# Performance work log

Hardware: AMD Instinct MI355X
Metric: run time of the kernel (lower is better)

Reference implementation:

```python
import jax, jax.numpy as jnp
import numpy as np
import math

HIDDEN = 1024
HEADS = 16
HEAD_DIM = HIDDEN // HEADS


def setup_inputs() -> dict:
    key = jax.random.key(0)
    k1, k2, k3, k4, k5 = jax.random.split(key, 5)
    B, S = 2, 2048
    scale = 1.0 / math.sqrt(HIDDEN)
    return {
        "batch_hidden": jax.random.normal(k1, (B, S, HIDDEN), dtype=jnp.float32),
        # nn.Linear weights are [out, in]; y = x @ W.T
        "Wq": jax.random.uniform(k2, (HIDDEN, HIDDEN), jnp.float32, -scale, scale),
        "Wk": jax.random.uniform(k3, (HIDDEN, HIDDEN), jnp.float32, -scale, scale),
        "Wg": jax.random.uniform(k4, (HIDDEN, HIDDEN), jnp.float32, -scale, scale),
        "bg": jax.random.uniform(k5, (HIDDEN,), jnp.float32, -scale, scale),
    }


def _split_heads(x):
    # [B,S,H] -> [B,heads,S,head_dim]
    B, S, _ = x.shape
    return x.reshape(B, S, HEADS, HEAD_DIM).transpose(0, 2, 1, 3)


def reference(batch_hidden, Wq, Wk, Wg, bg):
    # NOTE: faithful to source — value uses the KEY projection weights.
    q = batch_hidden @ Wq.T
    k = batch_hidden @ Wk.T
    v = batch_hidden @ Wk.T
    gate = jax.nn.sigmoid(batch_hidden @ Wg.T + bg)  # [B,S,H]

    q = _split_heads(q)  # [B,h,S,d]
    k = _split_heads(k)
    v = _split_heads(v)

    # source: scores = K @ Q^T (softmax over query positions)
    scores = jnp.einsum("bhkd,bhqd->bhkq", k, q) / math.sqrt(HEAD_DIM)
    attn = jax.nn.softmax(scores, axis=-1)  # [B,h,S,S]

    ctx = jnp.einsum("bhkq,bhqd->bhkd", attn, v)  # [B,h,S,d]
    ctx = ctx.transpose(0, 2, 1, 3).reshape(batch_hidden.shape)  # [B,S,H]

    out = gate * ctx
    return out, attn
```

## Files before the change

kernel.cpp:

```cpp
#include <hip/hip_runtime.h>
#include <hip/hip_bf16.h>

#define HID 1024
#define NHEADS 16
#define HDIM 64
#define SEQ 2048
#define NTOK 4096

typedef __attribute__((ext_vector_type(8))) short short8;
typedef __attribute__((ext_vector_type(4))) float f32x4;
typedef unsigned short ush;

__device__ __forceinline__ ush f2bf(float f) {
    unsigned int u = __float_as_uint(f);
    u = (u + 0x7fffu + ((u >> 16) & 1u)) >> 16;
    return (ush)u;
}
__device__ __forceinline__ void async_copy16(const void* g, void* l) {
    __builtin_amdgcn_global_load_lds(
        (const __attribute__((address_space(1))) void*)g,
        (__attribute__((address_space(3))) void*)l, 16, 0, 0);
}
#define SBAR()  __builtin_amdgcn_s_barrier()
#define SCHED() __builtin_amdgcn_sched_barrier(0)

__global__ __launch_bounds__(256) void cvt_kernel(
    const float* __restrict__ X, const float* __restrict__ Wq,
    const float* __restrict__ Wk, const float* __restrict__ Wg,
    ush* __restrict__ Xbf, ush* __restrict__ Wbf)
{
    long i = (long)blockIdx.x * 256 + threadIdx.x;
    const float* src; ush* dst; long j;
    if (i < 524288)      { src = X;  dst = Xbf;           j = i; }
    else if (i < 655360) { src = Wq; dst = Wbf;           j = i - 524288; }
    else if (i < 786432) { src = Wk; dst = Wbf + 1048576; j = i - 655360; }
    else                 { src = Wg; dst = Wbf + 2097152; j = i - 786432; }
    float4 a = *reinterpret_cast<const float4*>(src + j * 8);
    float4 b = *reinterpret_cast<const float4*>(src + j * 8 + 4);
    short8 o;
    o[0] = (short)f2bf(a.x); o[1] = (short)f2bf(a.y);
    o[2] = (short)f2bf(a.z); o[3] = (short)f2bf(a.w);
    o[4] = (short)f2bf(b.x); o[5] = (short)f2bf(b.y);
    o[6] = (short)f2bf(b.z); o[7] = (short)f2bf(b.w);
    *reinterpret_cast<short8*>(dst + j * 8) = o;
}

__global__ __launch_bounds__(256, 3) void proj_kernel(
    const ush* __restrict__ Xbf, const ush* __restrict__ Wbf,
    const float* __restrict__ bgp,
    ush* __restrict__ Qbf, ush* __restrict__ Kbf,
    ush* __restrict__ VtG,
    float* __restrict__ gate)
{
    __shared__ __align__(16) ush As[128 * 64];
    __shared__ __align__(16) ush Bs[128 * 64];

    const int lin = blockIdx.y * 24 + blockIdx.x;
    const int swz = (lin & 7) * 96 + (lin >> 3);
    const int n0 = (swz % 24) * 128;
    const int m0 = (swz / 24) * 128;
    const int tid = threadIdx.x, lane = tid & 63, wv = tid >> 6;
    const int wm = wv >> 1, wn = wv & 1;
    const int l16 = lane & 15, lq = lane >> 4;
    const int lrow = lane >> 3, lc = lane & 7;
    const int scU = lc ^ lrow;
    const int u0 = lq ^ (l16 & 7);

    f32x4 acc[4][4];
    #pragma unroll
    for (int i = 0; i < 4; i++)
        #pragma unroll
        for (int j = 0; j < 4; j++)
            #pragma unroll
            for (int r = 0; r < 4; r++) acc[i][j][r] = 0.0f;

    const ush* gA = Xbf + (long)m0 * HID;
    const ush* gB = Wbf + (long)n0 * HID;

    for (int k0 = 0; k0 < HID; k0 += 64) {
        #pragma unroll
        for (int c = 0; c < 4; ++c) {
            int chunk = wv * 4 + c;
            int row = chunk * 8 + lrow;
            async_copy16(gA + (long)row * HID + k0 + scU * 8, &As[chunk * 512]);
            async_copy16(gB + (long)row * HID + k0 + scU * 8, &Bs[chunk * 512]);
        }
        asm volatile("s_waitcnt vmcnt(0)" ::: "memory");
        SCHED();
        SBAR(); SCHED();
        #pragma unroll
        for (int ks = 0; ks < 2; ++ks) {
            const int uo = (ks ? (u0 ^ 4) : u0) * 8;
            short8 a[4], b[4];
            #pragma unroll
            for (int mf = 0; mf < 4; mf++)
                a[mf] = *reinterpret_cast<const short8*>(&As[(wm * 64 + mf * 16 + l16) * 64 + uo]);
            #pragma unroll
            for (int nf = 0; nf < 4; nf++)
                b[nf] = *reinterpret_cast<const short8*>(&Bs[(wn * 64 + nf * 16 + l16) * 64 + uo]);
            #pragma unroll
            for (int mf = 0; mf < 4; mf++)
                #pragma unroll
                for (int nf = 0; nf < 4; nf++)
                    acc[mf][nf] = __builtin_amdgcn_mfma_f32_16x16x32_bf16(a[mf], b[nf], acc[mf][nf], 0, 0, 0);
        }
        SBAR(); SCHED();
    }

    const int z = n0 >> 10;
    #pragma unroll
    for (int mf = 0; mf < 4; mf++)
        #pragma unroll
        for (int nf = 0; nf < 4; nf++) {
            int row = m0 + wm * 64 + mf * 16 + lq * 4;
            int gcol = n0 + wn * 64 + nf * 16 + l16;
            int col = gcol & 1023;
            #pragma unroll
            for (int r = 0; r < 4; r++) {
                float v = acc[mf][nf][r];
                long idx = (long)(row + r) * HID + col;
                if (z == 0)      Qbf[idx] = f2bf(v * 0.18033688011112042f);
                else if (z == 1) Kbf[idx] = f2bf(v);
                else {
                    float gv = 1.0f / (1.0f + __expf(-(v + bgp[col])));
                    __builtin_nontemporal_store(gv, &gate[idx]);
                }
            }
            if (z == 1) {
                int bb = row >> 11, s = row & 2047;
                int bh = bb * NHEADS + (col >> 6);
                int d  = col & 63;
                unsigned int w0, w1;
                asm volatile("v_cvt_pk_bf16_f32 %0, %1, %2" : "=v"(w0)
                             : "v"(acc[mf][nf][0]), "v"(acc[mf][nf][1]));
                asm volatile("v_cvt_pk_bf16_f32 %0, %1, %2" : "=v"(w1)
                             : "v"(acc[mf][nf][2]), "v"(acc[mf][nf][3]));
                *reinterpret_cast<uint2*>(&VtG[((long)bh * HDIM + d) * SEQ + s]) =
                    make_uint2(w0, w1);
            }
        }
}

__global__ __launch_bounds__(256, 2) void attn_kernel(
    const ush* __restrict__ Qbf,
    const ush* __restrict__ Kbf,
    const ush* __restrict__ VtG,
    float* __restrict__ outp,
    float* __restrict__ attnp)
{
    __shared__ __align__(16) ush Ks[128 * 64];
    __shared__ __align__(16) ush QsA[3 * 4096 + 128 * 72];
    __shared__ __align__(16) ush Vt[2][64 * 64];

    ush (*At)[72] = reinterpret_cast<ush(*)[72]>(&QsA[12288]);

    const int lin = (blockIdx.z * 16 + blockIdx.y) * 16 + blockIdx.x;
    const int swzb = (lin & 7) * 64 + (lin >> 3);
    const int kblk = swzb & 15;
    const int h    = (swzb >> 4) & 15;
    const int b    = swzb >> 8;
    const int bh   = b * NHEADS + h;
    const int tb   = b * SEQ;
    const int colbase = h * HDIM;
    const int tid  = threadIdx.x;
    const int lane = tid & 63;
    const int wv   = tid >> 6;
    const int l16  = lane & 15, lq = lane >> 4;
    const int lrow = lane >> 3, lc = lane & 7;
    const int scU  = lc ^ lrow;
    const int u0   = lq ^ (l16 & 7);

    const ush* Krow = Kbf + (long)(tb + kblk * 128) * HID + colbase;

    auto stageK = [&]() {
        #pragma unroll
        for (int c = 0; c < 4; ++c) {
            int chunk = wv * 4 + c;
            int row = chunk * 8 + lrow;
            async_copy16(Krow + (long)row * HID + scU * 8, &Ks[chunk * 512]);
        }
    };
    auto stageQ = [&](int q0, int bu) {
        #pragma unroll
        for (int c = 0; c < 2; ++c) {
            int chunk = wv * 2 + c;
            int row = chunk * 8 + lrow;
            async_copy16(Qbf + (long)(tb + q0 + row) * HID + colbase + scU * 8,
                         &QsA[bu * 4096 + chunk * 512]);
        }
    };
    auto stageV = [&](int q0, int bu) {
        #pragma unroll
        for (int c = 0; c < 2; ++c) {
            int chunk = wv * 2 + c;
            int row = chunk * 8 + lrow;
            async_copy16(VtG + ((long)bh * HDIM + row) * SEQ + q0 + scU * 8,
                         &Vt[bu][chunk * 512]);
        }
    };

    stageK();
    stageQ(0, 0);
    stageQ(64, 1);

    float ps[2] = {0.0f, 0.0f};

    for (int i = 0; i < 32; ++i) {
        if (i >= 30) asm volatile("s_waitcnt vmcnt(0)" ::: "memory");
        else         asm volatile("s_waitcnt vmcnt(2)" ::: "memory");
        SCHED();
        SBAR(); SCHED();
        if (i < 30) stageQ((i + 2) * 64, (i + 2) & 3);

        f32x4 acc[4][2];
        #pragma unroll
        for (int x = 0; x < 4; x++)
            #pragma unroll
            for (int y = 0; y < 2; y++)
                #pragma unroll
                for (int r = 0; r < 4; r++) acc[x][y][r] = 0.0f;

        const ush* Qb = &QsA[(i & 3) * 4096];
        #pragma unroll
        for (int ks = 0; ks < 2; ks++) {
            const int uo = (ks ? (u0 ^ 4) : u0) * 8;
            short8 aq[4], bk[2];
            #pragma unroll
            for (int mf = 0; mf < 4; mf++)
                aq[mf] = *reinterpret_cast<const short8*>(&Qb[(mf * 16 + l16) * 64 + uo]);
            #pragma unroll
            for (int nf = 0; nf < 2; nf++)
                bk[nf] = *reinterpret_cast<const short8*>(&Ks[(wv * 32 + nf * 16 + l16) * 64 + uo]);
            #pragma unroll
            for (int mf = 0; mf < 4; mf++)
                #pragma unroll
                for (int nf = 0; nf < 2; nf++)
                    acc[mf][nf] = __builtin_amdgcn_mfma_f32_16x16x32_bf16(aq[mf], bk[nf], acc[mf][nf], 0, 0, 0);
        }

        #pragma unroll
        for (int nf = 0; nf < 2; nf++) {
            float s = 0.0f;
            #pragma unroll
            for (int mf = 0; mf < 4; mf++)
                #pragma unroll
                for (int r = 0; r < 4; r++)
                    s += exp2f(acc[mf][nf][r]);
            ps[nf] += s;
        }
    }

    float inv_r[2];
    #pragma unroll
    for (int nf = 0; nf < 2; nf++) {
        float v = ps[nf];
        v += __shfl_xor(v, 16);
        v += __shfl_xor(v, 32);
        inv_r[nf] = 1.0f / v;
    }

    f32x4 octx[2][4];
    #pragma unroll
    for (int x = 0; x < 2; x++)
        #pragma unroll
        for (int y = 0; y < 4; y++)
            #pragma unroll
            for (int r = 0; r < 4; r++) octx[x][y][r] = 0.0f;

    SBAR();
    stageQ(0, 0); stageV(0, 0);
    stageQ(64, 1); stageV(64, 1);

    for (int i = 0; i < 32; ++i) {
        const int q0 = i << 6;
        if (i == 0)       asm volatile("s_waitcnt vmcnt(4)"  ::: "memory");
        else if (i == 1)  asm volatile("s_waitcnt vmcnt(12)" ::: "memory");
        else if (i == 31) asm volatile("s_waitcnt vmcnt(16)" ::: "memory");
        else              asm volatile("s_waitcnt vmcnt(20)" ::: "memory");
        SCHED();
        SBAR(); SCHED();
        if (i < 30) stageQ((i + 2) * 64, (i + 2) % 3);

        f32x4 acc[4][2];
        #pragma unroll
        for (int x = 0; x < 4; x++)
            #pragma unroll
            for (int y = 0; y < 2; y++)
                #pragma unroll
                for (int r = 0; r < 4; r++) acc[x][y][r] = 0.0f;

        const ush* Qb = &QsA[(i % 3) * 4096];
        #pragma unroll
        for (int ks = 0; ks < 2; ks++) {
            const int uo = (ks ? (u0 ^ 4) : u0) * 8;
            short8 aq[4], bk[2];
            #pragma unroll
            for (int mf = 0; mf < 4; mf++)
                aq[mf] = *reinterpret_cast<const short8*>(&Qb[(mf * 16 + l16) * 64 + uo]);
            #pragma unroll
            for (int nf = 0; nf < 2; nf++)
                bk[nf] = *reinterpret_cast<const short8*>(&Ks[(wv * 32 + nf * 16 + l16) * 64 + uo]);
            #pragma unroll
            for (int mf = 0; mf < 4; mf++)
                #pragma unroll
                for (int nf = 0; nf < 2; nf++)
                    acc[mf][nf] = __builtin_amdgcn_mfma_f32_16x16x32_bf16(aq[mf], bk[nf], acc[mf][nf], 0, 0, 0);
        }

        #pragma unroll
        for (int nf = 0; nf < 2; nf++) {
            const int krl = wv * 32 + nf * 16 + l16;
            const float inv = inv_r[nf];
            #pragma unroll
            for (int mf = 0; mf < 4; mf++) {
                const int qc = mf * 16 + lq * 4;
                float p0 = exp2f(acc[mf][nf][0]) * inv;
                float p1 = exp2f(acc[mf][nf][1]) * inv;
                float p2 = exp2f(acc[mf][nf][2]) * inv;
                float p3 = exp2f(acc[mf][nf][3]) * inv;
                unsigned int w0, w1;
                asm volatile("v_cvt_pk_bf16_f32 %0, %1, %2" : "=v"(w0) : "v"(p0), "v"(p1));
                asm volatile("v_cvt_pk_bf16_f32 %0, %1, %2" : "=v"(w1) : "v"(p2), "v"(p3));
                *reinterpret_cast<uint2*>(&At[krl][qc]) = make_uint2(w0, w1);
            }
        }

        asm volatile("s_waitcnt lgkmcnt(0)" ::: "memory");
        SCHED();

        uint2 wreg[8];
        const int rlo = lane >> 4;
        const int qc  = (lane & 15) * 4;
        #pragma unroll
        for (int j = 0; j < 8; ++j)
            wreg[j] = *reinterpret_cast<const uint2*>(&At[wv * 32 + j * 4 + rlo][qc]);

        #pragma unroll
        for (int ks = 0; ks < 2; ks++) {
            const int uo = (ks ? (u0 ^ 4) : u0) * 8;
            short8 a[2], bv[4];
            #pragma unroll
            for (int mf = 0; mf < 2; mf++)
                a[mf] = *reinterpret_cast<const short8*>(&At[wv * 32 + mf * 16 + l16][ks * 32 + lq * 8]);
            #pragma unroll
            for (int nf = 0; nf < 4; nf++)
                bv[nf] = *reinterpret_cast<const short8*>(&Vt[i & 1][(nf * 16 + l16) * 64 + uo]);
            #pragma unroll
            for (int mf = 0; mf < 2; mf++)
                #pragma unroll
                for (int nf = 0; nf < 4; nf++)
                    octx[mf][nf] = __builtin_amdgcn_mfma_f32_16x16x32_bf16(a[mf], bv[nf], octx[mf][nf], 0, 0, 0);
        }

        SBAR(); SCHED();
        if (i < 30) stageV((i + 2) * 64, i & 1);

        #pragma unroll
        for (int j = 0; j < 8; ++j) {
            const int rl = wv * 32 + j * 4 + rlo;
            f32x4 st;
            st[0] = __uint_as_float(wreg[j].x << 16);
            st[1] = __uint_as_float(wreg[j].x & 0xffff0000u);
            st[2] = __uint_as_float(wreg[j].y << 16);
            st[3] = __uint_as_float(wreg[j].y & 0xffff0000u);
            __builtin_nontemporal_store(st,
                reinterpret_cast<f32x4*>(attnp + ((long)bh * SEQ + kblk * 128 + rl) * SEQ + q0 + qc));
        }
    }

    #pragma unroll
    for (int mf = 0; mf < 2; mf++)
        #pragma unroll
        for (int nf = 0; nf < 4; nf++) {
            int row = tb + kblk * 128 + wv * 32 + mf * 16 + lq * 4;
            int col = colbase + nf * 16 + l16;
            #pragma unroll
            for (int r = 0; r < 4; r++) {
                long idx = (long)(row + r) * HID + col;
                float g = __builtin_nontemporal_load(&outp[idx]);
                __builtin_nontemporal_store(g * octx[mf][nf][r], &outp[idx]);
            }
        }
}

extern "C" void kernel_launch(void* const* d_in, const int* in_sizes, int n_in,
                              void* d_out, int out_size, void* d_ws, size_t ws_size,
                              hipStream_t stream)
{
    const float* X  = (const float*)d_in[0];
    const float* Wq = (const float*)d_in[1];
    const float* Wk = (const float*)d_in[2];
    const float* Wg = (const float*)d_in[3];
    const float* bg = (const float*)d_in[4];

    float* outp  = (float*)d_out;
    float* attnp = outp + (long)NTOK * HID;

    ush* Qbf = (ush*)d_ws;
    ush* Kbf = Qbf + (long)NTOK * HID;
    ush* VtG = Kbf + (long)NTOK * HID;

    ush* Xbf = (ush*)(outp + 134742016L);
    ush* Wbf = Xbf + (long)NTOK * HID;

    cvt_kernel<<<3584, 256, 0, stream>>>(X, Wq, Wk, Wg, Xbf, Wbf);
    proj_kernel<<<dim3(24, 32), 256, 0, stream>>>(Xbf, Wbf, bg, Qbf, Kbf, VtG, outp);
    attn_kernel<<<dim3(16, 16, 2), 256, 0, stream>>>(Qbf, Kbf, VtG, outp, attnp);
}
```

Measured before the change: 216.5 us.

## Cut attention LDS footprint to fit three blocks per CU, keep K in registers

```diff
diff --git a/kernel.cpp b/kernel.cpp
--- a/kernel.cpp
+++ b/kernel.cpp
@@ -141,18 +141,18 @@
         }
 }
 
-__global__ __launch_bounds__(256, 2) void attn_kernel(
+__global__ __launch_bounds__(256, 3) void attn_kernel(
     const ush* __restrict__ Qbf,
     const ush* __restrict__ Kbf,
     const ush* __restrict__ VtG,
     float* __restrict__ outp,
     float* __restrict__ attnp)
 {
-    __shared__ __align__(16) ush Ks[128 * 64];
-    __shared__ __align__(16) ush QsA[3 * 4096 + 128 * 72];
-    __shared__ __align__(16) ush Vt[2][64 * 64];
-
-    ush (*At)[72] = reinterpret_cast<ush(*)[72]>(&QsA[12288]);
+    __shared__ __align__(16) ush QsA[3 * 4096];
+    __shared__ __align__(16) ush AtA[128 * 72];
+    __shared__ __align__(16) ush VtA[64 * 64];
+
+    ush (*At)[72] = reinterpret_cast<ush(*)[72]>(&AtA[0]);
 
     const int lin = (blockIdx.z * 16 + blockIdx.y) * 16 + blockIdx.x;
     const int swzb = (lin & 7) * 64 + (lin >> 3);
@@ -172,14 +172,6 @@
 
     const ush* Krow = Kbf + (long)(tb + kblk * 128) * HID + colbase;
 
-    auto stageK = [&]() {
-        #pragma unroll
-        for (int c = 0; c < 4; ++c) {
-            int chunk = wv * 4 + c;
-            int row = chunk * 8 + lrow;
-            async_copy16(Krow + (long)row * HID + scU * 8, &Ks[chunk * 512]);
-        }
-    };
     auto stageQ = [&](int q0, int bu) {
         #pragma unroll
         for (int c = 0; c < 2; ++c) {
@@ -189,17 +181,38 @@
                          &QsA[bu * 4096 + chunk * 512]);
         }
     };
-    auto stageV = [&](int q0, int bu) {
+    auto stageV = [&](int q0) {
         #pragma unroll
         for (int c = 0; c < 2; ++c) {
             int chunk = wv * 2 + c;
             int row = chunk * 8 + lrow;
             async_copy16(VtG + ((long)bh * HDIM + row) * SEQ + q0 + scU * 8,
-                         &Vt[bu][chunk * 512]);
+                         &VtA[chunk * 512]);
         }
     };
 
-    stageK();
+    short8 bk[2][2];
+    {
+        #pragma unroll
+        for (int c = 0; c < 4; ++c) {
+            int chunk = wv * 4 + c;
+            int row = chunk * 8 + lrow;
+            async_copy16(Krow + (long)row * HID + scU * 8, &AtA[chunk * 512]);
+        }
+        asm volatile("s_waitcnt vmcnt(0)" ::: "memory");
+        SCHED();
+        SBAR(); SCHED();
+        #pragma unroll
+        for (int ks = 0; ks < 2; ++ks) {
+            const int uo = (ks ? (u0 ^ 4) : u0) * 8;
+            #pragma unroll
+            for (int nf = 0; nf < 2; ++nf)
+                bk[ks][nf] = *reinterpret_cast<const short8*>(
+                    &AtA[(wv * 32 + nf * 16 + l16) * 64 + uo]);
+        }
+        SBAR(); SCHED();
+    }
+
     stageQ(0, 0);
     stageQ(64, 1);
 
@@ -210,7 +223,7 @@
         else         asm volatile("s_waitcnt vmcnt(2)" ::: "memory");
         SCHED();
         SBAR(); SCHED();
-        if (i < 30) stageQ((i + 2) * 64, (i + 2) & 3);
+        if (i < 30) stageQ((i + 2) * 64, (i + 2) % 3);
 
         f32x4 acc[4][2];
         #pragma unroll
@@ -220,23 +233,22 @@
                 #pragma unroll
                 for (int r = 0; r < 4; r++) acc[x][y][r] = 0.0f;
 
-        const ush* Qb = &QsA[(i & 3) * 4096];
+        const ush* Qb = &QsA[(i % 3) * 4096];
+        __builtin_amdgcn_s_setprio(1);
         #pragma unroll
         for (int ks = 0; ks < 2; ks++) {
             const int uo = (ks ? (u0 ^ 4) : u0) * 8;
-            short8 aq[4], bk[2];
+            short8 aq[4];
             #pragma unroll
             for (int mf = 0; mf < 4; mf++)
                 aq[mf] = *reinterpret_cast<const short8*>(&Qb[(mf * 16 + l16) * 64 + uo]);
             #pragma unroll
-            for (int nf = 0; nf < 2; nf++)
-                bk[nf] = *reinterpret_cast<const short8*>(&Ks[(wv * 32 + nf * 16 + l16) * 64 + uo]);
-            #pragma unroll
             for (int mf = 0; mf < 4; mf++)
                 #pragma unroll
                 for (int nf = 0; nf < 2; nf++)
-                    acc[mf][nf] = __builtin_amdgcn_mfma_f32_16x16x32_bf16(aq[mf], bk[nf], acc[mf][nf], 0, 0, 0);
-        }
+                    acc[mf][nf] = __builtin_amdgcn_mfma_f32_16x16x32_bf16(aq[mf], bk[ks][nf], acc[mf][nf], 0, 0, 0);
+        }
+        __builtin_amdgcn_s_setprio(0);
 
         #pragma unroll
         for (int nf = 0; nf < 2; nf++) {
@@ -268,15 +280,14 @@
             for (int r = 0; r < 4; r++) octx[x][y][r] = 0.0f;
 
     SBAR();
-    stageQ(0, 0); stageV(0, 0);
-    stageQ(64, 1); stageV(64, 1);
+    stageQ(0, 0);
+    stageV(0);
+    stageQ(64, 1);
 
     for (int i = 0; i < 32; ++i) {
         const int q0 = i << 6;
-        if (i == 0)       asm volatile("s_waitcnt vmcnt(4)"  ::: "memory");
-        else if (i == 1)  asm volatile("s_waitcnt vmcnt(12)" ::: "memory");
-        else if (i == 31) asm volatile("s_waitcnt vmcnt(16)" ::: "memory");
-        else              asm volatile("s_waitcnt vmcnt(20)" ::: "memory");
+        if (i == 0) asm volatile("s_waitcnt vmcnt(2)" ::: "memory");
+        else        asm volatile("s_waitcnt vmcnt(8)" ::: "memory");
         SCHED();
         SBAR(); SCHED();
         if (i < 30) stageQ((i + 2) * 64, (i + 2) % 3);
@@ -290,22 +301,21 @@
                 for (int r = 0; r < 4; r++) acc[x][y][r] = 0.0f;
 
         const ush* Qb = &QsA[(i % 3) * 4096];
+        __builtin_amdgcn_s_setprio(1);
         #pragma unroll
         for (int ks = 0; ks < 2; ks++) {
             const int uo = (ks ? (u0 ^ 4) : u0) * 8;
-            short8 aq[4], bk[2];
+            short8 aq[4];
             #pragma unroll
             for (int mf = 0; mf < 4; mf++)
                 aq[mf] = *reinterpret_cast<const short8*>(&Qb[(mf * 16 + l16) * 64 + uo]);
             #pragma unroll
-            for (int nf = 0; nf < 2; nf++)
-                bk[nf] = *reinterpret_cast<const short8*>(&Ks[(wv * 32 + nf * 16 + l16) * 64 + uo]);
-            #pragma unroll
             for (int mf = 0; mf < 4; mf++)
                 #pragma unroll
                 for (int nf = 0; nf < 2; nf++)
-                    acc[mf][nf] = __builtin_amdgcn_mfma_f32_16x16x32_bf16(aq[mf], bk[nf], acc[mf][nf], 0, 0, 0);
-        }
+                    acc[mf][nf] = __builtin_amdgcn_mfma_f32_16x16x32_bf16(aq[mf], bk[ks][nf], acc[mf][nf], 0, 0, 0);
+        }
+        __builtin_amdgcn_s_setprio(0);
 
         #pragma unroll
         for (int nf = 0; nf < 2; nf++) {
@@ -335,6 +345,7 @@
         for (int j = 0; j < 8; ++j)
             wreg[j] = *reinterpret_cast<const uint2*>(&At[wv * 32 + j * 4 + rlo][qc]);
 
+        __builtin_amdgcn_s_setprio(1);
         #pragma unroll
         for (int ks = 0; ks < 2; ks++) {
             const int uo = (ks ? (u0 ^ 4) : u0) * 8;
@@ -344,16 +355,17 @@
                 a[mf] = *reinterpret_cast<const short8*>(&At[wv * 32 + mf * 16 + l16][ks * 32 + lq * 8]);
             #pragma unroll
             for (int nf = 0; nf < 4; nf++)
-                bv[nf] = *reinterpret_cast<const short8*>(&Vt[i & 1][(nf * 16 + l16) * 64 + uo]);
+                bv[nf] = *reinterpret_cast<const short8*>(&VtA[(nf * 16 + l16) * 64 + uo]);
             #pragma unroll
             for (int mf = 0; mf < 2; mf++)
                 #pragma unroll
                 for (int nf = 0; nf < 4; nf++)
                     octx[mf][nf] = __builtin_amdgcn_mfma_f32_16x16x32_bf16(a[mf], bv[nf], octx[mf][nf], 0, 0, 0);
         }
-
-        SBAR(); SCHED();
-        if (i < 30) stageV((i + 2) * 64, i & 1);
+        __builtin_amdgcn_s_setprio(0);
+
+        SBAR(); SCHED();
+        if (i < 31) stageV((i + 1) * 64);
 
         #pragma unroll
         for (int j = 0; j < 8; ++j) {
```

New measurement: 214.2 us. No clear change (-1.0%).
